# Kernel tuning notes

Hardware: AMD Instinct MI355X
Metric: run time of the kernel (lower is better)

Reference implementation:

```python
import jax, jax.numpy as jnp
import numpy as np

B, I, J, DIN, DOUT = 256, 1152, 10, 8, 16
ROUTING_ITERS = 3


def squash(v):
    # v: [..., D]; squash(v) = (|v|^2 / (1+|v|^2)) * v/|v| = v * |v| / (1+|v|^2)
    l2 = jnp.linalg.norm(v, axis=-1, keepdims=True)
    return v * (l2 / (1.0 + l2 * l2))


def setup_inputs() -> dict:
    key = jax.random.key(0)
    k1, k2 = jax.random.split(key)
    x = jax.random.normal(k1, (B, I, DIN), dtype=jnp.float32)
    # per-(i,j) Linear(DIN -> DOUT, bias=False) weights, stacked: [I, J, DOUT, DIN]
    W = jax.random.normal(k2, (I, J, DOUT, DIN), dtype=jnp.float32) * 0.1
    return {"x": x, "W": W}


def reference(x, W):
    # prediction vectors u[b,i,j,:] = W[i,j] @ x[b,i,:]  -> [B, I, J, DOUT]
    u = jnp.einsum('bid,ijod->bijo', x, W)
    b = jnp.zeros((I, J), dtype=u.dtype)  # routing logits (shared across batch)
    s = None
    for _ in range(ROUTING_ITERS):
        c = jax.nn.softmax(b, axis=-1)              # [I, J]
        s = jnp.einsum('ij,bijd->bjd', c, u)        # coupling-weighted sum over in-caps
        s = squash(s)                               # [B, J, DOUT]
        # agreement: b[i,j] += sum_b <u[b,i,j], s[b,j]>
        b = b + jnp.einsum('bijd,bjd->ij', u, s)
    return s
```

## Files before the change

kernel.cpp:

```cpp
#include <hip/hip_runtime.h>
#include <math.h>

typedef unsigned short ushort_t;
typedef __attribute__((ext_vector_type(8))) __bf16 bf16x8;
typedef __attribute__((ext_vector_type(4))) float floatx4;

#define B_    256
#define I_    1152
#define J_    10
#define DIN_  8
#define DOUT_ 16
#define K_    (I_*DIN_)
#define N_    (J_*DOUT_)
#define KSPLIT 16
#define KCHUNK (K_/KSPLIT)
#define KSTEPS (KCHUNK/32)
#define CHUNK16 2368

static __device__ __forceinline__ ushort_t f2bf(float f) {
    unsigned int u = __float_as_uint(f);
    u += 0x7fffu + ((u >> 16) & 1u);
    return (ushort_t)(u >> 16);
}
static __device__ __forceinline__ float bf2f(ushort_t h) {
    return __uint_as_float(((unsigned int)h) << 16);
}

__global__ __launch_bounds__(256)
void prep_all_kernel(const float* __restrict__ x, const float* __restrict__ W,
                     ushort_t* __restrict__ xPk, float* __restrict__ wPk)
{
    const int blk = blockIdx.x;
    const int tid = threadIdx.x;

    if (blk < 1152) {
        const int gid = blk * 256 + tid;
        const int f   = gid * 8;
        const int row = f / K_;
        const int kk  = f - row * K_;
        const int kc  = kk / KCHUNK;
        const int t   = kk - kc * KCHUNK;
        const int s   = t >> 5;
        const int q   = (t & 31) >> 3;
        const int mb  = row >> 4, r = row & 15;

        const float* src = x + (size_t)f;
        bf16x8 h8, l8;
        #pragma unroll
        for (int e = 0; e < 8; ++e) {
            float v = src[e];
            __bf16 h = (__bf16)v;
            h8[e] = h;
            l8[e] = (__bf16)(v - (float)h);
        }
        bf16x8* dst = (bf16x8*)xPk + (size_t)(mb * 16 + kc) * CHUNK16 + s * 128 + q * 16 + r;
        dst[0]  = h8;
        dst[64] = l8;
    } else {
        const int gid = (blk - 1152) * 256 + tid;
        const int f   = gid * 4;
        const int i   = f / 1280;
        const int rem = f - i * 1280;
        const int no  = rem >> 3;
        const int p   = (rem >> 2) & 1;
        const int nt  = no >> 4, r = no & 15;
        const int kc  = i / 72;
        const int m   = i - kc * 72;
        const int s   = m >> 2, q = m & 3;
        float4 v = *(const float4*)(W + (size_t)f);
        ((float4*)wPk)[(size_t)(nt * 16 + kc) * CHUNK16 + (s * 2 + p) * 64 + q * 16 + r] = v;
    }
}

__global__ __launch_bounds__(256)
void gemm_s_part_kernel(const ushort_t* __restrict__ xPk, const float* __restrict__ wPk,
                        const float* __restrict__ blog,
                        float* __restrict__ pbuf, const int iter)
{
    const int tid   = threadIdx.x;
    const int blk   = blockIdx.x;
    const int kb    = blk & 7;
    const int tile  = blk >> 3;
    const int mb    = tile & 15;
    const int nt    = tile >> 4;
    const int lane  = tid & 63;
    const int w     = tid >> 6;
    const int kc    = kb * 2 + (w >> 1);
    const int shalf = w & 1;

    __shared__ float   c_lds[144];
    __shared__ floatx4 part[4 * 64];

    if (iter > 0) {
        for (int r2 = tid; r2 < 144; r2 += 256) {
            const float* br = blog + (size_t)(kb * 144 + r2) * J_;
            float bv[J_];
            float mx = -1e30f;
            #pragma unroll
            for (int j = 0; j < J_; ++j) { bv[j] = br[j]; mx = fmaxf(mx, bv[j]); }
            float sum = 0.f;
            #pragma unroll
            for (int j = 0; j < J_; ++j) { bv[j] = __expf(bv[j] - mx); sum += bv[j]; }
            c_lds[r2] = bv[nt] / sum;
        }
        __syncthreads();
    }

    {
        const int q = lane >> 4;
        const int sbase = shalf * 9;
        const bf16x8* xp = (const bf16x8*)xPk + (size_t)(mb * 16 + kc) * CHUNK16
                           + sbase * 128 + lane;
        const float4* wp = (const float4*)wPk + (size_t)(nt * 16 + kc) * CHUNK16
                           + sbase * 128 + lane;
        floatx4 acc = {0.f, 0.f, 0.f, 0.f};

        bf16x8 rah[2], ral[2];
        float4 rw0[2], rw1[2];
        #pragma unroll
        for (int s = 0; s < 2; ++s) {
            rah[s] = xp[s * 128];
            ral[s] = xp[s * 128 + 64];
            rw0[s] = wp[s * 128];
            rw1[s] = wp[s * 128 + 64];
        }
        #pragma unroll
        for (int s = 0; s < 9; ++s) {
            bf16x8 ah = rah[s & 1], al = ral[s & 1];
            float4 w0 = rw0[s & 1], w1 = rw1[s & 1];
            if (s + 2 < 9) {
                rah[s & 1] = xp[(s + 2) * 128];
                ral[s & 1] = xp[(s + 2) * 128 + 64];
                rw0[s & 1] = wp[(s + 2) * 128];
                rw1[s & 1] = wp[(s + 2) * 128 + 64];
            }
            float cs = (iter == 0) ? 0.1f
                                   : c_lds[(w >> 1) * 72 + 4 * (sbase + s) + q];
            float wvv[8] = {w0.x, w0.y, w0.z, w0.w, w1.x, w1.y, w1.z, w1.w};
            bf16x8 bh, bl;
            #pragma unroll
            for (int e = 0; e < 8; ++e) {
                float pe = wvv[e] * cs;
                __bf16 g = (__bf16)pe;
                bh[e] = g;
                bl[e] = (__bf16)(pe - (float)g);
            }
            acc = __builtin_amdgcn_mfma_f32_16x16x32_bf16(ah, bh, acc, 0, 0, 0);
            acc = __builtin_amdgcn_mfma_f32_16x16x32_bf16(al, bh, acc, 0, 0, 0);
            acc = __builtin_amdgcn_mfma_f32_16x16x32_bf16(ah, bl, acc, 0, 0, 0);
        }
        part[w * 64 + lane] = acc;
    }
    __syncthreads();

    const int row = tid >> 4;
    const int o   = tid & 15;
    const int lane_c = ((row >> 2) << 4) | o;
    const int reg    = row & 3;
    float v = part[0 * 64 + lane_c][reg] + part[1 * 64 + lane_c][reg]
            + part[2 * 64 + lane_c][reg] + part[3 * 64 + lane_c][reg];
    pbuf[(size_t)blk * 256 + row * 16 + o] = v;
}

__global__ __launch_bounds__(256)
void reduce_squash_kernel(const float* __restrict__ pbuf, float* __restrict__ s_out,
                          ushort_t* __restrict__ Sbt_hi, ushort_t* __restrict__ Sbt_lo,
                          const int iter)
{
    const int tile = blockIdx.x;
    const int mb   = tile & 15;
    const int nt   = tile >> 4;
    const int t    = threadIdx.x;
    const int row  = t >> 4;
    const int o    = t & 15;

    const float* pb = pbuf + (size_t)tile * 8 * 256 + row * 16 + o;
    float v = 0.f;
    #pragma unroll
    for (int u = 0; u < 8; ++u)
        v += pb[u * 256];

    float sq = v * v;
    #pragma unroll
    for (int off = 1; off < 16; off <<= 1)
        sq += __shfl_xor(sq, off, 16);
    float l2 = sqrtf(sq);
    float val = v * (l2 / (1.f + sq));
    const int b  = mb * 16 + row;
    const int jo = nt * 16 + o;
    if (iter == 2) {
        s_out[(size_t)b * N_ + jo] = val;
    } else {
        ushort_t hi = f2bf(val);
        Sbt_hi[(size_t)jo * B_ + b] = hi;
        Sbt_lo[(size_t)jo * B_ + b] = f2bf(val - bf2f(hi));
    }
}

__global__ __launch_bounds__(256)
void gemm_bupd_kernel(const float* __restrict__ x,
                      const ushort_t* __restrict__ Sbt_hi, const ushort_t* __restrict__ Sbt_lo,
                      const float* __restrict__ W, float* __restrict__ blog,
                      const int first)
{
    int wv   = (blockIdx.x & 7) * 360 + (blockIdx.x >> 3) * 4 + (threadIdx.x >> 6);
    int lane = threadIdx.x & 63;
    int mt = wv / 5;
    int jp = wv - mt * 5;
    int j0 = jp * 2, j1 = jp * 2 + 1;
    int r = lane & 15, q = lane >> 4;
    const float* xp = x + (size_t)(8 * q) * K_ + (mt * 16 + r);
    size_t b0off = (size_t)(j0 * 16 + r) * B_ + 8 * q;
    size_t b1off = (size_t)(j1 * 16 + r) * B_ + 8 * q;
    floatx4 acc0 = {0.f, 0.f, 0.f, 0.f};
    floatx4 acc1 = {0.f, 0.f, 0.f, 0.f};

    float xcur[8], xnxt[8];
    #pragma unroll
    for (int e = 0; e < 8; ++e) xcur[e] = xp[(size_t)e * K_];
    #pragma unroll
    for (int s = 0; s < B_ / 32; ++s) {
        if (s + 1 < B_ / 32) {
            #pragma unroll
            for (int e = 0; e < 8; ++e)
                xnxt[e] = xp[(size_t)((s + 1) * 32 + e) * K_];
        }
        bf16x8 ah, al;
        #pragma unroll
        for (int e = 0; e < 8; ++e) {
            float v = xcur[e];
            __bf16 h = (__bf16)v;
            ah[e] = h;
            al[e] = (__bf16)(v - (float)h);
        }
        bf16x8 bh0 = *(const bf16x8*)(Sbt_hi + b0off + s * 32);
        bf16x8 bl0 = *(const bf16x8*)(Sbt_lo + b0off + s * 32);
        bf16x8 bh1 = *(const bf16x8*)(Sbt_hi + b1off + s * 32);
        bf16x8 bl1 = *(const bf16x8*)(Sbt_lo + b1off + s * 32);
        acc0 = __builtin_amdgcn_mfma_f32_16x16x32_bf16(ah, bh0, acc0, 0, 0, 0);
        acc0 = __builtin_amdgcn_mfma_f32_16x16x32_bf16(al, bh0, acc0, 0, 0, 0);
        acc0 = __builtin_amdgcn_mfma_f32_16x16x32_bf16(ah, bl0, acc0, 0, 0, 0);
        acc1 = __builtin_amdgcn_mfma_f32_16x16x32_bf16(ah, bh1, acc1, 0, 0, 0);
        acc1 = __builtin_amdgcn_mfma_f32_16x16x32_bf16(al, bh1, acc1, 0, 0, 0);
        acc1 = __builtin_amdgcn_mfma_f32_16x16x32_bf16(ah, bl1, acc1, 0, 0, 0);
        #pragma unroll
        for (int e = 0; e < 8; ++e) xcur[e] = xnxt[e];
    }
    int i  = mt * 2 + (q >> 1);
    int d0 = (q & 1) * 4;
    int o  = lane & 15;
    int iw = mt * 2 + (lane >> 5);
    {
        const float4 w4 = *(const float4*)(W + ((((size_t)i * J_ + j0) * DOUT_ + o) * DIN_ + d0));
        float val = acc0[0] * w4.x + acc0[1] * w4.y + acc0[2] * w4.z + acc0[3] * w4.w;
        #pragma unroll
        for (int off = 1; off < 32; off <<= 1)
            val += __shfl_xor(val, off, 32);
        if ((lane & 31) == 0) {
            float* dst = blog + (size_t)iw * J_ + j0;
            if (first) *dst = val; else *dst += val;
        }
    }
    {
        const float4 w4 = *(const float4*)(W + ((((size_t)i * J_ + j1) * DOUT_ + o) * DIN_ + d0));
        float val = acc1[0] * w4.x + acc1[1] * w4.y + acc1[2] * w4.z + acc1[3] * w4.w;
        #pragma unroll
        for (int off = 1; off < 32; off <<= 1)
            val += __shfl_xor(val, off, 32);
        if ((lane & 31) == 0) {
            float* dst = blog + (size_t)iw * J_ + j1;
            if (first) *dst = val; else *dst += val;
        }
    }
}

extern "C" void kernel_launch(void* const* d_in, const int* in_sizes, int n_in,
                              void* d_out, int out_size, void* d_ws, size_t ws_size,
                              hipStream_t stream)
{
    const float* x = (const float*)d_in[0];
    const float* W = (const float*)d_in[1];
    float* s_out = (float*)d_out;

    char* ws = (char*)d_ws;
    ushort_t* Sbt_hi = (ushort_t*)(ws);
    ushort_t* Sbt_lo = (ushort_t*)(ws + 81920);
    float*    blog   = (float*)   (ws + 163840);
    float*    pbuf   = (float*)   (ws + 262144);
    ushort_t* xPk    = (ushort_t*)(ws + 1572864);
    float*    wPk    = (float*)   (ws + 11272192);

    prep_all_kernel<<<2592, 256, 0, stream>>>(x, W, xPk, wPk);

    for (int it = 0; it < 3; ++it) {
        gemm_s_part_kernel<<<1280, 256, 0, stream>>>(xPk, wPk, blog, pbuf, it);
        reduce_squash_kernel<<<160, 256, 0, stream>>>(pbuf, s_out,
                                                      Sbt_hi, Sbt_lo, it);
        if (it < 2)
            gemm_bupd_kernel<<<720, 256, 0, stream>>>(x, Sbt_hi, Sbt_lo,
                                                      W, blog, it == 0 ? 1 : 0);
    }
}
```

Measured before the change: 135.5 us.

## Fuse split-K reduce/squash into GEMM via last-block counters and overlap prep

```diff
diff --git a/kernel.cpp b/kernel.cpp
--- a/kernel.cpp
+++ b/kernel.cpp
@@ -25,57 +25,175 @@
 static __device__ __forceinline__ float bf2f(ushort_t h) {
     return __uint_as_float(((unsigned int)h) << 16);
 }
+static __device__ __forceinline__ void ast_f(float* p, float v) {
+    __hip_atomic_store(p, v, __ATOMIC_RELAXED, __HIP_MEMORY_SCOPE_AGENT);
+}
+static __device__ __forceinline__ float ald_f(const float* p) {
+    return __hip_atomic_load(p, __ATOMIC_RELAXED, __HIP_MEMORY_SCOPE_AGENT);
+}
+
+static __device__ __forceinline__
+void ab_epilogue(float* __restrict__ pbuf_it, unsigned int* __restrict__ cnt_it,
+                 float* __restrict__ s_out, ushort_t* __restrict__ Sbt_hi,
+                 ushort_t* __restrict__ Sbt_lo, const floatx4* part, int* last_s,
+                 int tile, int kb, int mb, int nt, int tid, int it)
+{
+    const int row = tid >> 4;
+    const int o   = tid & 15;
+    const int lane_c = ((row >> 2) << 4) | o;
+    const int reg    = row & 3;
+    float v = part[0 * 64 + lane_c][reg] + part[1 * 64 + lane_c][reg]
+            + part[2 * 64 + lane_c][reg] + part[3 * 64 + lane_c][reg];
+    ast_f(pbuf_it + (size_t)(tile * 8 + kb) * 256 + row * 16 + o, v);
+    __syncthreads();
+    if (tid == 0)
+        *last_s = (atomicAdd(cnt_it + tile, 1u) == 7u);
+    __syncthreads();
+    if (!*last_s) return;
+
+    const float* pb = pbuf_it + (size_t)tile * 8 * 256 + row * 16 + o;
+    float vv = 0.f;
+    #pragma unroll
+    for (int u = 0; u < 8; ++u)
+        vv += ald_f(pb + u * 256);
+    float sq = vv * vv;
+    #pragma unroll
+    for (int off = 1; off < 16; off <<= 1)
+        sq += __shfl_xor(sq, off, 16);
+    float l2 = sqrtf(sq);
+    float val = vv * (l2 / (1.f + sq));
+    const int b  = mb * 16 + row;
+    const int jo = nt * 16 + o;
+    if (it == 2) {
+        s_out[(size_t)b * N_ + jo] = val;
+    } else {
+        ushort_t hi = f2bf(val);
+        Sbt_hi[(size_t)jo * B_ + b] = hi;
+        Sbt_lo[(size_t)jo * B_ + b] = f2bf(val - bf2f(hi));
+    }
+}
 
 __global__ __launch_bounds__(256)
-void prep_all_kernel(const float* __restrict__ x, const float* __restrict__ W,
-                     ushort_t* __restrict__ xPk, float* __restrict__ wPk)
+void d1_kernel(const float* __restrict__ x, const float* __restrict__ W,
+               ushort_t* __restrict__ xPk, float* __restrict__ wPk,
+               float* __restrict__ pbuf, unsigned int* __restrict__ cnt,
+               float* __restrict__ s_out,
+               ushort_t* __restrict__ Sbt_hi, ushort_t* __restrict__ Sbt_lo)
 {
     const int blk = blockIdx.x;
     const int tid = threadIdx.x;
 
-    if (blk < 1152) {
-        const int gid = blk * 256 + tid;
-        const int f   = gid * 8;
-        const int row = f / K_;
-        const int kk  = f - row * K_;
-        const int kc  = kk / KCHUNK;
-        const int t   = kk - kc * KCHUNK;
-        const int s   = t >> 5;
-        const int q   = (t & 31) >> 3;
-        const int mb  = row >> 4, r = row & 15;
-
-        const float* src = x + (size_t)f;
-        bf16x8 h8, l8;
-        #pragma unroll
-        for (int e = 0; e < 8; ++e) {
-            float v = src[e];
-            __bf16 h = (__bf16)v;
-            h8[e] = h;
-            l8[e] = (__bf16)(v - (float)h);
-        }
-        bf16x8* dst = (bf16x8*)xPk + (size_t)(mb * 16 + kc) * CHUNK16 + s * 128 + q * 16 + r;
-        dst[0]  = h8;
-        dst[64] = l8;
-    } else {
-        const int gid = (blk - 1152) * 256 + tid;
-        const int f   = gid * 4;
-        const int i   = f / 1280;
-        const int rem = f - i * 1280;
-        const int no  = rem >> 3;
-        const int p   = (rem >> 2) & 1;
-        const int nt  = no >> 4, r = no & 15;
-        const int kc  = i / 72;
-        const int m   = i - kc * 72;
-        const int s   = m >> 2, q = m & 3;
-        float4 v = *(const float4*)(W + (size_t)f);
-        ((float4*)wPk)[(size_t)(nt * 16 + kc) * CHUNK16 + (s * 2 + p) * 64 + q * 16 + r] = v;
-    }
+    if (blk >= 1280) {
+        if (blk < 2432) {
+            const int gid = (blk - 1280) * 256 + tid;
+            const int f   = gid * 8;
+            const int row = f / K_;
+            const int kk  = f - row * K_;
+            const int kc  = kk / KCHUNK;
+            const int t   = kk - kc * KCHUNK;
+            const int s   = t >> 5;
+            const int q   = (t & 31) >> 3;
+            const int mb  = row >> 4, r = row & 15;
+            const float* src = x + (size_t)f;
+            bf16x8 h8, l8;
+            #pragma unroll
+            for (int e = 0; e < 8; ++e) {
+                float v = src[e];
+                __bf16 h = (__bf16)v;
+                h8[e] = h;
+                l8[e] = (__bf16)(v - (float)h);
+            }
+            bf16x8* dst = (bf16x8*)xPk + (size_t)(mb * 16 + kc) * CHUNK16 + s * 128 + q * 16 + r;
+            dst[0]  = h8;
+            dst[64] = l8;
+        } else {
+            const int gid = (blk - 2432) * 256 + tid;
+            const int f   = gid * 4;
+            const int i   = f / 1280;
+            const int rem = f - i * 1280;
+            const int no  = rem >> 3;
+            const int p   = (rem >> 2) & 1;
+            const int nt  = no >> 4, r = no & 15;
+            const int kc  = i / 72;
+            const int m   = i - kc * 72;
+            const int s   = m >> 2, q = m & 3;
+            float4 v = *(const float4*)(W + (size_t)f);
+            ((float4*)wPk)[(size_t)(nt * 16 + kc) * CHUNK16 + (s * 2 + p) * 64 + q * 16 + r] = v;
+        }
+        return;
+    }
+
+    const int kb    = blk & 7;
+    const int tile  = blk >> 3;
+    const int mb    = tile & 15;
+    const int nt    = tile >> 4;
+    const int lane  = tid & 63;
+    const int w     = tid >> 6;
+    const int kc    = kb * 2 + (w >> 1);
+    const int sbase = (w & 1) * 9;
+
+    __shared__ floatx4 part[4 * 64];
+    __shared__ int     last_s;
+
+    {
+        const int r = lane & 15, q = lane >> 4;
+        const float* ap = x + (size_t)(mb * 16 + r) * K_ + kc * KCHUNK + 8 * q + sbase * 32;
+        const float* wp = W + (((size_t)(kc * 72 + q) * J_ + nt) * DOUT_ + r) * DIN_;
+        const size_t wstep = (size_t)4 * J_ * DOUT_ * DIN_;
+        const float* wps = wp + sbase * wstep;
+        floatx4 acc = {0.f, 0.f, 0.f, 0.f};
+
+        float4 bxa0[2], bxa1[2], bw0[2], bw1[2];
+        #pragma unroll
+        for (int s = 0; s < 2; ++s) {
+            bxa0[s] = *(const float4*)(ap + s * 32);
+            bxa1[s] = *(const float4*)(ap + s * 32 + 4);
+            bw0[s]  = *(const float4*)(wps + s * wstep);
+            bw1[s]  = *(const float4*)(wps + s * wstep + 4);
+        }
+        #pragma unroll
+        for (int s = 0; s < 9; ++s) {
+            float4 xa0 = bxa0[s & 1], xa1 = bxa1[s & 1];
+            float4 w0  = bw0[s & 1],  w1  = bw1[s & 1];
+            if (s + 2 < 9) {
+                bxa0[s & 1] = *(const float4*)(ap + (s + 2) * 32);
+                bxa1[s & 1] = *(const float4*)(ap + (s + 2) * 32 + 4);
+                bw0[s & 1]  = *(const float4*)(wps + (s + 2) * wstep);
+                bw1[s & 1]  = *(const float4*)(wps + (s + 2) * wstep + 4);
+            }
+            const float cs = 0.1f;
+            float xv[8]  = {xa0.x, xa0.y, xa0.z, xa0.w, xa1.x, xa1.y, xa1.z, xa1.w};
+            float wvv[8] = {w0.x, w0.y, w0.z, w0.w, w1.x, w1.y, w1.z, w1.w};
+            bf16x8 ah, al, bh, bl;
+            #pragma unroll
+            for (int e = 0; e < 8; ++e) {
+                float xe = xv[e];
+                __bf16 h = (__bf16)xe;
+                ah[e] = h;
+                al[e] = (__bf16)(xe - (float)h);
+                float pe = wvv[e] * cs;
+                __bf16 g = (__bf16)pe;
+                bh[e] = g;
+                bl[e] = (__bf16)(pe - (float)g);
+            }
+            acc = __builtin_amdgcn_mfma_f32_16x16x32_bf16(ah, bh, acc, 0, 0, 0);
+            acc = __builtin_amdgcn_mfma_f32_16x16x32_bf16(al, bh, acc, 0, 0, 0);
+            acc = __builtin_amdgcn_mfma_f32_16x16x32_bf16(ah, bl, acc, 0, 0, 0);
+        }
+        part[w * 64 + lane] = acc;
+    }
+    __syncthreads();
+    ab_epilogue(pbuf, cnt, s_out, Sbt_hi, Sbt_lo, part, &last_s,
+                tile, kb, mb, nt, tid, 0);
 }
 
 __global__ __launch_bounds__(256)
-void gemm_s_part_kernel(const ushort_t* __restrict__ xPk, const float* __restrict__ wPk,
-                        const float* __restrict__ blog,
-                        float* __restrict__ pbuf, const int iter)
+void gemm_s_ab_kernel(const ushort_t* __restrict__ xPk, const float* __restrict__ wPk,
+                      const float* __restrict__ blog,
+                      float* __restrict__ pbuf, unsigned int* __restrict__ cnt,
+                      float* __restrict__ s_out,
+                      ushort_t* __restrict__ Sbt_hi, ushort_t* __restrict__ Sbt_lo,
+                      const int iter)
 {
     const int tid   = threadIdx.x;
     const int blk   = blockIdx.x;
@@ -90,8 +208,9 @@
 
     __shared__ float   c_lds[144];
     __shared__ floatx4 part[4 * 64];
-
-    if (iter > 0) {
+    __shared__ int     last_s;
+
+    {
         for (int r2 = tid; r2 < 144; r2 += 256) {
             const float* br = blog + (size_t)(kb * 144 + r2) * J_;
             float bv[J_];
@@ -134,8 +253,7 @@
                 rw0[s & 1] = wp[(s + 2) * 128];
                 rw1[s & 1] = wp[(s + 2) * 128 + 64];
             }
-            float cs = (iter == 0) ? 0.1f
-                                   : c_lds[(w >> 1) * 72 + 4 * (sbase + s) + q];
+            float cs = c_lds[(w >> 1) * 72 + 4 * (sbase + s) + q];
             float wvv[8] = {w0.x, w0.y, w0.z, w0.w, w1.x, w1.y, w1.z, w1.w};
             bf16x8 bh, bl;
             #pragma unroll
@@ -152,49 +270,8 @@
         part[w * 64 + lane] = acc;
     }
     __syncthreads();
-
-    const int row = tid >> 4;
-    const int o   = tid & 15;
-    const int lane_c = ((row >> 2) << 4) | o;
-    const int reg    = row & 3;
-    float v = part[0 * 64 + lane_c][reg] + part[1 * 64 + lane_c][reg]
-            + part[2 * 64 + lane_c][reg] + part[3 * 64 + lane_c][reg];
-    pbuf[(size_t)blk * 256 + row * 16 + o] = v;
-}
-
-__global__ __launch_bounds__(256)
-void reduce_squash_kernel(const float* __restrict__ pbuf, float* __restrict__ s_out,
-                          ushort_t* __restrict__ Sbt_hi, ushort_t* __restrict__ Sbt_lo,
-                          const int iter)
-{
-    const int tile = blockIdx.x;
-    const int mb   = tile & 15;
-    const int nt   = tile >> 4;
-    const int t    = threadIdx.x;
-    const int row  = t >> 4;
-    const int o    = t & 15;
-
-    const float* pb = pbuf + (size_t)tile * 8 * 256 + row * 16 + o;
-    float v = 0.f;
-    #pragma unroll
-    for (int u = 0; u < 8; ++u)
-        v += pb[u * 256];
-
-    float sq = v * v;
-    #pragma unroll
-    for (int off = 1; off < 16; off <<= 1)
-        sq += __shfl_xor(sq, off, 16);
-    float l2 = sqrtf(sq);
-    float val = v * (l2 / (1.f + sq));
-    const int b  = mb * 16 + row;
-    const int jo = nt * 16 + o;
-    if (iter == 2) {
-        s_out[(size_t)b * N_ + jo] = val;
-    } else {
-        ushort_t hi = f2bf(val);
-        Sbt_hi[(size_t)jo * B_ + b] = hi;
-        Sbt_lo[(size_t)jo * B_ + b] = f2bf(val - bf2f(hi));
-    }
+    ab_epilogue(pbuf, cnt, s_out, Sbt_hi, Sbt_lo, part, &last_s,
+                tile, kb, mb, nt, tid, iter);
 }
 
 __global__ __launch_bounds__(256)
@@ -283,21 +360,24 @@
     float* s_out = (float*)d_out;
 
     char* ws = (char*)d_ws;
-    ushort_t* Sbt_hi = (ushort_t*)(ws);
-    ushort_t* Sbt_lo = (ushort_t*)(ws + 81920);
-    float*    blog   = (float*)   (ws + 163840);
-    float*    pbuf   = (float*)   (ws + 262144);
-    ushort_t* xPk    = (ushort_t*)(ws + 1572864);
-    float*    wPk    = (float*)   (ws + 11272192);
-
-    prep_all_kernel<<<2592, 256, 0, stream>>>(x, W, xPk, wPk);
-
-    for (int it = 0; it < 3; ++it) {
-        gemm_s_part_kernel<<<1280, 256, 0, stream>>>(xPk, wPk, blog, pbuf, it);
-        reduce_squash_kernel<<<160, 256, 0, stream>>>(pbuf, s_out,
-                                                      Sbt_hi, Sbt_lo, it);
-        if (it < 2)
-            gemm_bupd_kernel<<<720, 256, 0, stream>>>(x, Sbt_hi, Sbt_lo,
-                                                      W, blog, it == 0 ? 1 : 0);
-    }
-}
+    ushort_t*     Sbt_hi = (ushort_t*)(ws);
+    ushort_t*     Sbt_lo = (ushort_t*)(ws + 81920);
+    float*        blog   = (float*)   (ws + 163840);
+    float*        pbuf   = (float*)   (ws + 262144);
+    ushort_t*     xPk    = (ushort_t*)(ws + 4194304);
+    float*        wPk    = (float*)   (ws + 13893632);
+    unsigned int* cnt    = (unsigned int*)(ws + 19955712);
+
+    (void)hipMemsetAsync(ws + 19955712, 0, 1920, stream);
+
+    d1_kernel<<<3872, 256, 0, stream>>>(x, W, xPk, wPk,
+                                        pbuf, cnt, s_out, Sbt_hi, Sbt_lo);
+    gemm_bupd_kernel<<<720, 256, 0, stream>>>(x, Sbt_hi, Sbt_lo, W, blog, 1);
+    gemm_s_ab_kernel<<<1280, 256, 0, stream>>>(xPk, wPk, blog,
+                                               pbuf + 327680, cnt + 160,
+                                               s_out, Sbt_hi, Sbt_lo, 1);
+    gemm_bupd_kernel<<<720, 256, 0, stream>>>(x, Sbt_hi, Sbt_lo, W, blog, 0);
+    gemm_s_ab_kernel<<<1280, 256, 0, stream>>>(xPk, wPk, blog,
+                                               pbuf + 655360, cnt + 320,
+                                               s_out, Sbt_hi, Sbt_lo, 2);
+}
```

Measured after the change: 140.6 us. +3.7%, slower.

## Fuse split-K reduction and squash into GEMM via last-block atomic counter

Applied to the files above, without the earlier changes.

```diff
diff --git a/kernel.cpp b/kernel.cpp
--- a/kernel.cpp
+++ b/kernel.cpp
@@ -25,13 +25,24 @@
 static __device__ __forceinline__ float bf2f(ushort_t h) {
     return __uint_as_float(((unsigned int)h) << 16);
 }
+static __device__ __forceinline__ void ast_f(float* p, float v) {
+    __hip_atomic_store(p, v, __ATOMIC_RELAXED, __HIP_MEMORY_SCOPE_AGENT);
+}
+static __device__ __forceinline__ float ald_f(const float* p) {
+    return __hip_atomic_load(p, __ATOMIC_RELAXED, __HIP_MEMORY_SCOPE_AGENT);
+}
 
 __global__ __launch_bounds__(256)
 void prep_all_kernel(const float* __restrict__ x, const float* __restrict__ W,
-                     ushort_t* __restrict__ xPk, float* __restrict__ wPk)
+                     ushort_t* __restrict__ xPk, float* __restrict__ wPk,
+                     unsigned int* __restrict__ cnt)
 {
     const int blk = blockIdx.x;
     const int tid = threadIdx.x;
+
+    if (blk == 0) {
+        for (int i = tid; i < 480; i += 256) cnt[i] = 0u;
+    }
 
     if (blk < 1152) {
         const int gid = blk * 256 + tid;
@@ -73,9 +84,12 @@
 }
 
 __global__ __launch_bounds__(256)
-void gemm_s_part_kernel(const ushort_t* __restrict__ xPk, const float* __restrict__ wPk,
-                        const float* __restrict__ blog,
-                        float* __restrict__ pbuf, const int iter)
+void gemm_s_ab_kernel(const ushort_t* __restrict__ xPk, const float* __restrict__ wPk,
+                      const float* __restrict__ blog,
+                      float* __restrict__ pbuf_it, unsigned int* __restrict__ cnt_it,
+                      float* __restrict__ s_out,
+                      ushort_t* __restrict__ Sbt_hi, ushort_t* __restrict__ Sbt_lo,
+                      const int iter)
 {
     const int tid   = threadIdx.x;
     const int blk   = blockIdx.x;
@@ -90,6 +104,7 @@
 
     __shared__ float   c_lds[144];
     __shared__ floatx4 part[4 * 64];
+    __shared__ int     last_s;
 
     if (iter > 0) {
         for (int r2 = tid; r2 < 144; r2 += 256) {
@@ -159,33 +174,24 @@
     const int reg    = row & 3;
     float v = part[0 * 64 + lane_c][reg] + part[1 * 64 + lane_c][reg]
             + part[2 * 64 + lane_c][reg] + part[3 * 64 + lane_c][reg];
-    pbuf[(size_t)blk * 256 + row * 16 + o] = v;
-}
-
-__global__ __launch_bounds__(256)
-void reduce_squash_kernel(const float* __restrict__ pbuf, float* __restrict__ s_out,
-                          ushort_t* __restrict__ Sbt_hi, ushort_t* __restrict__ Sbt_lo,
-                          const int iter)
-{
-    const int tile = blockIdx.x;
-    const int mb   = tile & 15;
-    const int nt   = tile >> 4;
-    const int t    = threadIdx.x;
-    const int row  = t >> 4;
-    const int o    = t & 15;
-
-    const float* pb = pbuf + (size_t)tile * 8 * 256 + row * 16 + o;
-    float v = 0.f;
+    ast_f(pbuf_it + (size_t)(tile * 8 + kb) * 256 + row * 16 + o, v);
+    __syncthreads();
+    if (tid == 0)
+        last_s = (atomicAdd(cnt_it + tile, 1u) == 7u);
+    __syncthreads();
+    if (!last_s) return;
+
+    const float* pb = pbuf_it + (size_t)tile * 8 * 256 + row * 16 + o;
+    float vv = 0.f;
     #pragma unroll
     for (int u = 0; u < 8; ++u)
-        v += pb[u * 256];
-
-    float sq = v * v;
+        vv += ald_f(pb + u * 256);
+    float sq = vv * vv;
     #pragma unroll
     for (int off = 1; off < 16; off <<= 1)
         sq += __shfl_xor(sq, off, 16);
     float l2 = sqrtf(sq);
-    float val = v * (l2 / (1.f + sq));
+    float val = vv * (l2 / (1.f + sq));
     const int b  = mb * 16 + row;
     const int jo = nt * 16 + o;
     if (iter == 2) {
@@ -283,19 +289,21 @@
     float* s_out = (float*)d_out;
 
     char* ws = (char*)d_ws;
-    ushort_t* Sbt_hi = (ushort_t*)(ws);
-    ushort_t* Sbt_lo = (ushort_t*)(ws + 81920);
-    float*    blog   = (float*)   (ws + 163840);
-    float*    pbuf   = (float*)   (ws + 262144);
-    ushort_t* xPk    = (ushort_t*)(ws + 1572864);
-    float*    wPk    = (float*)   (ws + 11272192);
-
-    prep_all_kernel<<<2592, 256, 0, stream>>>(x, W, xPk, wPk);
+    ushort_t*     Sbt_hi = (ushort_t*)(ws);
+    ushort_t*     Sbt_lo = (ushort_t*)(ws + 81920);
+    float*        blog   = (float*)   (ws + 163840);
+    float*        pbuf   = (float*)   (ws + 262144);
+    unsigned int* cnt    = (unsigned int*)(ws + 4194304);
+    ushort_t*     xPk    = (ushort_t*)(ws + 4196352);
+    float*        wPk    = (float*)   (ws + 13895680);
+
+    prep_all_kernel<<<2592, 256, 0, stream>>>(x, W, xPk, wPk, cnt);
 
     for (int it = 0; it < 3; ++it) {
-        gemm_s_part_kernel<<<1280, 256, 0, stream>>>(xPk, wPk, blog, pbuf, it);
-        reduce_squash_kernel<<<160, 256, 0, stream>>>(pbuf, s_out,
-                                                      Sbt_hi, Sbt_lo, it);
+        gemm_s_ab_kernel<<<1280, 256, 0, stream>>>(xPk, wPk, blog,
+                                                   pbuf + (size_t)it * 327680,
+                                                   cnt + it * 160,
+                                                   s_out, Sbt_hi, Sbt_lo, it);
         if (it < 2)
             gemm_bupd_kernel<<<720, 256, 0, stream>>>(x, Sbt_hi, Sbt_lo,
                                                       W, blog, it == 0 ? 1 : 0);
```

New measurement: 136.7 us. No clear change (+0.9%).
